# Kernel optimization log

Hardware: AMD Instinct MI355X
Metric: run time of the kernel (lower is better)

## Reference

```python
import jax, jax.numpy as jnp
import numpy as np

HIDDEN = 256
TOPK = 16
SINK_BLOCKS = 5
TAU = 1.0
SOFT_ALPHA = 8.0
LN_EPS = 1e-5


def setup_inputs() -> dict:
    key = jax.random.key(0)
    ks = jax.random.split(key, 8)
    B, T, QD, KD, J = 2, 1024, 1024, 1024, 64
    H = HIDDEN
    H3 = 3 * H
    s = 0.02
    return {
        "Q": jax.random.normal(ks[0], (B, T, QD), dtype=jnp.float32),
        "K": jax.random.normal(ks[1], (B, J, KD), dtype=jnp.float32),
        "Wq": jax.random.normal(ks[2], (H, QD), dtype=jnp.float32) * s,
        "Wk": jax.random.normal(ks[3], (H, KD), dtype=jnp.float32) * s,
        "ln_g": jnp.ones((H3,), dtype=jnp.float32),
        "ln_b": jnp.zeros((H3,), dtype=jnp.float32),
        "Wu": jax.random.normal(ks[4], (H, H3), dtype=jnp.float32) * s,
        "bu": jnp.zeros((H,), dtype=jnp.float32),
        "Wv": jax.random.normal(ks[5], (H, H3), dtype=jnp.float32) * s,
        "bv": jnp.zeros((H,), dtype=jnp.float32),
        "Wo": jax.random.normal(ks[6], (1, H), dtype=jnp.float32) * s,
        "bo": jnp.zeros((1,), dtype=jnp.float32),
        "chunk_len": 16,
        "L_ctx": 1024,
    }


def _forward(Q, K, Wq, Wk, ln_g, ln_b, Wu, bu, Wv, bv, Wo, bo, chunk_len, L_ctx):
    B, T, _ = Q.shape
    J = K.shape[1]
    # ---- GatedScorer ----
    q = jnp.einsum('btd,hd->bth', Q, Wq)  # (B,T,H)
    k = jnp.einsum('bjd,hd->bjh', K, Wk)  # (B,J,H)
    H = q.shape[-1]
    qb = jnp.broadcast_to(q[:, :, None, :], (B, T, J, H))
    kb = jnp.broadcast_to(k[:, None, :, :], (B, T, J, H))
    x = jnp.concatenate([qb, kb, qb * kb], axis=-1)  # (B,T,J,3H)
    mu = jnp.mean(x, axis=-1, keepdims=True)
    var = jnp.mean((x - mu) ** 2, axis=-1, keepdims=True)
    x = (x - mu) / jnp.sqrt(var + LN_EPS) * ln_g + ln_b
    U = jnp.einsum('btjc,hc->btjh', x, Wu) + bu
    V = jnp.einsum('btjc,hc->btjh', x, Wv) + bv
    Z = U * jax.nn.gelu(V, approximate=False)
    logits = jnp.einsum('btjh,oh->btjo', Z, Wo)[..., 0] + bo[0]  # (B,T,J)

    # ---- top-k chunk selection (deterministic path, use_learnable_k=False) ----
    sink = int(min(max(0, SINK_BLOCKS), J))
    J_tail = J - sink
    topk_main = max(min(J, TOPK) - sink, 0)
    logits_tail = logits[..., sink:]  # (B,T,J_tail)
    causal = jnp.arange(J_tail)[None, :] <= jnp.arange(T)[:, None]  # tril(T,J_tail)
    masked = jnp.where(causal[None], logits_tail, -jnp.inf)
    _, idx_tail = jax.lax.top_k(masked, topk_main)
    idx_tail = idx_tail + sink
    sink_idx = jnp.broadcast_to(jnp.arange(sink)[None, None, :], (B, T, sink))
    idx = jnp.concatenate([sink_idx, idx_tail], axis=-1)  # (B,T,sink+topk_main)

    # ---- soft warmup weights ----
    w_soft = jax.nn.softmax(logits / TAU, axis=-1)  # (B,T,J)

    # ---- build_block_bias_from_topk ----
    num_chunks = (L_ctx + chunk_len - 1) // chunk_len
    sel = jnp.zeros((B, T, num_chunks), dtype=bool)
    sel = sel.at[jnp.arange(B)[:, None, None], jnp.arange(T)[None, :, None], idx].set(True)
    token_chunk = jnp.clip(jnp.arange(L_ctx) // chunk_len, 0, num_chunks - 1)  # (L_ctx,)
    sel_tok = jnp.take(sel, token_chunk, axis=-1)  # (B,T,L_ctx)
    per_chunk_bias = -SOFT_ALPHA * (1.0 - w_soft)  # (B,T,J)
    bias = jnp.take(per_chunk_bias, token_chunk, axis=-1)  # (B,T,L_ctx)
    bias = jnp.where(sel_tok, 0.0, bias)
    tri = jnp.arange(L_ctx)[None, :] > jnp.arange(T)[:, None]  # triu(T,L_ctx, diag=1)
    bias = jnp.where(tri[None], -jnp.inf, bias)
    return logits, bias


def reference(Q, K, Wq, Wk, ln_g, ln_b, Wu, bu, Wv, bv, Wo, bo, chunk_len, L_ctx):
    return _forward(Q, K, Wq, Wk, ln_g, ln_b, Wu, bu, Wv, bv, Wo, bo, chunk_len, L_ctx)
```

## Files before the change

kernel.cpp:

```cpp
#include <hip/hip_runtime.h>
#include <hip/hip_bf16.h>
#include <math.h>

#define H3 768

#define OFF_Q     0u
#define OFF_K     524288u
#define OFF_UVK   557056u
#define OFF_SQ    622592u
#define OFF_SQ2   624768u
#define OFF_WGU   626944u
#define OFF_WGV   627200u
#define OFF_CU    627456u
#define OFF_CV    627712u

#define BO_UVQ   0u
#define BO_WQF   1048576u
#define BO_WKF   1310720u
#define BO_BPK   1572864u
#define BO_WQBF  1703936u
#define BO_WKBF  1835008u

typedef __attribute__((ext_vector_type(8))) short bf16x8;
typedef __attribute__((ext_vector_type(4))) float f32x4;

__device__ __forceinline__ float bf2f(short s) {
    return __uint_as_float(((unsigned)(unsigned short)s) << 16);
}
union bfu { __hip_bfloat162 h; short2 s; };
__device__ __forceinline__ void split2(float a, float b, short* hi2, short* lo2) {
    bfu h; h.h = __float22bfloat162_rn(float2{a, b});
    float fa = bf2f(h.s.x), fb = bf2f(h.s.y);
    bfu l; l.h = __float22bfloat162_rn(float2{a - fa, b - fb});
    hi2[0] = h.s.x; hi2[1] = h.s.y;
    lo2[0] = l.s.x; lo2[1] = l.s.y;
}
__device__ __forceinline__ void split8(const float* v, bf16x8* vh, bf16x8* vl) {
    short h2[2], l2[2];
#pragma unroll
    for (int i = 0; i < 4; i++) {
        split2(v[2 * i], v[2 * i + 1], h2, l2);
        (*vh)[2 * i] = h2[0]; (*vh)[2 * i + 1] = h2[1];
        (*vl)[2 * i] = l2[0]; (*vl)[2 * i + 1] = l2[1];
    }
}

__device__ __forceinline__ float gelu_fast(float v) {
    float ar = v * 0.70710678118654752440f;
    float a = fabsf(ar);
    float t = __builtin_amdgcn_rcpf(fmaf(0.3275911f, a, 1.0f));
    float p = fmaf(fmaf(fmaf(fmaf(1.061405429f, t, -1.453152027f), t,
                             1.421413741f), t, -0.284496736f), t, 0.254829592f) * t;
    float e = __expf(-ar * ar);
    float er = fmaf(-p, e, 1.0f);
    er = copysignf(er, ar);
    return 0.5f * v * (1.0f + er);
}

__device__ __forceinline__ float wave_reduce_add(float v) {
#pragma unroll
    for (int off = 32; off > 0; off >>= 1) v += __shfl_xor(v, off, 64);
    return v;
}

__global__ __launch_bounds__(256) void prep(const float* __restrict__ Wq,
                                            const float* __restrict__ Wk,
                                            const float* __restrict__ Wu,
                                            const float* __restrict__ Wv,
                                            const float* __restrict__ g,
                                            const float* __restrict__ lb,
                                            const float* __restrict__ bu,
                                            const float* __restrict__ bv,
                                            float* __restrict__ ws,
                                            float* __restrict__ bsc) {
    int tid = threadIdx.x;
    int bid = blockIdx.x;
    if (bid >= 512) {
        ws[(bid - 512) * 256 + tid] = 0.0f;
        return;
    }
    if (bid < 64) {
        int h = bid * 4 + (tid >> 6);
        int lane = tid & 63;
        float su = 0.f, sv = 0.f, tu = 0.f, tv = 0.f;
#pragma unroll
        for (int i = 0; i < 12; i++) {
            int c = lane + 64 * i;
            float gg = g[c], bb = lb[c];
            float wu = Wu[h * H3 + c], wv = Wv[h * H3 + c];
            su += wu * gg; sv += wv * gg; tu += wu * bb; tv += wv * bb;
        }
        su = wave_reduce_add(su); sv = wave_reduce_add(sv);
        tu = wave_reduce_add(tu); tv = wave_reduce_add(tv);
        if (lane == 0) {
            ws[OFF_WGU + h] = su; ws[OFF_WGV + h] = sv;
            ws[OFF_CU + h] = tu + bu[h]; ws[OFF_CV + h] = tv + bv[h];
        }
        return;
    }
    float v8[8];
    bf16x8 vh, vl;
    if (bid < 320) {
        const float* W; bf16x8* dst;
        int idx;
        if (bid < 192) { idx = (bid - 64) * 256 + tid; W = Wq; dst = (bf16x8*)(bsc + BO_WQF); }
        else { idx = (bid - 192) * 256 + tid; W = Wk; dst = (bf16x8*)(bsc + BO_WKF); }
        int n = idx >> 7, k8 = idx & 127;
        const float* src = W + (size_t)n * 1024 + k8 * 8;
        *(float4*)&v8[0] = *(const float4*)src;
        *(float4*)&v8[4] = *(const float4*)(src + 4);
        split8(v8, &vh, &vl);
        int kc = k8 >> 2, grp = k8 & 3, lane = grp * 16 + (n & 15), ntg = n >> 4;
        size_t s0 = ((size_t)(kc * 16 + ntg) * 2) * 64 + lane;
        dst[s0] = vh; dst[s0 + 64] = vl;
        return;
    }
    int idx, c0;
    bf16x8* dst;
    int n;
    if (bid < 384) {
        idx = (bid - 320) * 256 + tid;
        n = idx >> 5; c0 = (idx & 31) * 8;
        dst = (bf16x8*)(bsc + BO_WQBF);
    } else if (bid < 448) {
        idx = (bid - 384) * 256 + tid;
        n = idx >> 5; c0 = 256 + (idx & 31) * 8;
        dst = (bf16x8*)(bsc + BO_WKBF);
    } else {
        idx = (bid - 448) * 256 + tid;
        n = idx >> 5; c0 = 512 + (idx & 31) * 8;
        dst = (bf16x8*)(bsc + BO_BPK);
    }
    int h, uv;
    if (bid < 448) { uv = (n < 256) ? 0 : 1; h = (n < 256) ? n : n - 256; }
    else {
        int ntg0 = n >> 4, cc = n & 15;
        uv = ntg0 & 1;
        h = ((ntg0 >> 3) << 6) | (((ntg0 >> 1) & 3) << 4) | cc;
    }
    const float* W = uv ? Wv : Wu;
#pragma unroll
    for (int i = 0; i < 8; i++) v8[i] = W[(size_t)h * H3 + c0 + i] * g[c0 + i];
    split8(v8, &vh, &vl);
    int k8 = (c0 & 255) >> 3;
    int kc = k8 >> 2, grp = k8 & 3, lane = grp * 16 + (n & 15), ntg = n >> 4;
    size_t s0 = ((size_t)(kc * 32 + ntg) * 2) * 64 + lane;
    dst[s0] = vh; dst[s0 + 64] = vl;
}

__global__ __launch_bounds__(256) void proj_mfma(const float* __restrict__ Q,
                                                 const float* __restrict__ Kin,
                                                 const float* __restrict__ bsc,
                                                 float* __restrict__ ws) {
    __shared__ __align__(16) short Ah[2][32 * 40], Al[2][32 * 40];
    int tid = threadIdx.x, bx = blockIdx.x, by = blockIdx.y, ks = blockIdx.z;
    const float* A; float* C; const bf16x8* BF;
    if (by < 64) {
        A = Q + (size_t)by * 32 * 1024;
        C = ws + OFF_Q + (size_t)by * 32 * 256;
        BF = (const bf16x8*)(bsc + BO_WQF);
    } else {
        A = Kin + (size_t)(by - 64) * 32 * 1024;
        C = ws + OFF_K + (size_t)(by - 64) * 32 * 256;
        BF = (const bf16x8*)(bsc + BO_WKF);
    }
    int w = tid >> 6, l = tid & 63, c15 = l & 15, grp = l >> 4;
    int mt = w & 1, np = w >> 1;
    int srow = tid >> 3, scol = (tid & 7) * 4;
    const float* arow = A + (size_t)srow * 1024 + ks * 512 + scol;
    f32x4 acc[2];
    acc[0] = (f32x4){0.f, 0.f, 0.f, 0.f};
    acc[1] = (f32x4){0.f, 0.f, 0.f, 0.f};
    float4 a4 = *(const float4*)&arow[0];
    for (int kc = 0; kc < 16; kc++) {
        int pb = kc & 1;
        short h4[4], l4[4];
        split2(a4.x, a4.y, &h4[0], &l4[0]);
        split2(a4.z, a4.w, &h4[2], &l4[2]);
        int ao = srow * 40 + scol;
        *(short4*)&Ah[pb][ao] = *(short4*)&h4[0];
        *(short4*)&Al[pb][ao] = *(short4*)&l4[0];
        if (kc < 15) a4 = *(const float4*)&arow[(kc + 1) * 32];
        __syncthreads();
        int fo = (mt * 16 + c15) * 40 + grp * 8;
        bf16x8 afh = *(const bf16x8*)&Ah[pb][fo];
        bf16x8 afl = *(const bf16x8*)&Al[pb][fo];
        int kcg = ks * 16 + kc;
        bf16x8 bh[2], bl[2];
#pragma unroll
        for (int i = 0; i < 2; i++) {
            int ntg = bx * 4 + 2 * np + i;
            size_t fi = ((size_t)(kcg * 16 + ntg) * 2) * 64 + l;
            bh[i] = BF[fi]; bl[i] = BF[fi + 64];
        }
#pragma unroll
        for (int i = 0; i < 2; i++)
            acc[i] = __builtin_amdgcn_mfma_f32_16x16x32_bf16(afl, bh[i], acc[i], 0, 0, 0);
#pragma unroll
        for (int i = 0; i < 2; i++)
            acc[i] = __builtin_amdgcn_mfma_f32_16x16x32_bf16(afh, bl[i], acc[i], 0, 0, 0);
#pragma unroll
        for (int i = 0; i < 2; i++)
            acc[i] = __builtin_amdgcn_mfma_f32_16x16x32_bf16(afh, bh[i], acc[i], 0, 0, 0);
    }
#pragma unroll
    for (int r = 0; r < 4; r++) {
        int rloc = mt * 16 + grp * 4 + r;
#pragma unroll
        for (int i = 0; i < 2; i++)
            atomicAdd(&C[(size_t)rloc * 256 + bx * 64 + (2 * np + i) * 16 + c15], acc[i][r]);
    }
}

__global__ __launch_bounds__(256) void uv_mfma(float* __restrict__ ws,
                                               float* __restrict__ bsc) {
    __shared__ __align__(16) short Ah[64 * 40], Al[64 * 40];
    int tid = threadIdx.x, bx = blockIdx.x, by = blockIdx.y;
    const float* A; float* C; const bf16x8* BF; int sbase;
    if (by < 32) {
        A = ws + OFF_Q + (size_t)by * 64 * 256;
        C = bsc + BO_UVQ + (size_t)by * 64 * 512;
        BF = (const bf16x8*)(bsc + BO_WQBF);
        sbase = by * 64;
    } else {
        A = ws + OFF_K + (size_t)(by - 32) * 64 * 256;
        C = ws + OFF_UVK + (size_t)(by - 32) * 64 * 512;
        BF = (const bf16x8*)(bsc + BO_WKBF);
        sbase = 2048 + (by - 32) * 64;
    }
    int w = tid >> 6, l = tid & 63, c15 = l & 15, grp = l >> 4;
    int srow = tid >> 2, scol = (tid & 3) * 8;
    f32x4 acc[4];
#pragma unroll
    for (int nt = 0; nt < 4; nt++) acc[nt] = (f32x4){0.f, 0.f, 0.f, 0.f};
    float s1 = 0.f, s2 = 0.f;
    for (int kc = 0; kc < 8; kc++) {
        float v8[8];
        const float* src = &A[(size_t)srow * 256 + kc * 32 + scol];
        *(float4*)&v8[0] = *(const float4*)src;
        *(float4*)&v8[4] = *(const float4*)(src + 4);
        if (bx == 0) {
#pragma unroll
            for (int i = 0; i < 8; i++) { s1 += v8[i]; s2 = fmaf(v8[i], v8[i], s2); }
        }
        bf16x8 vh, vl;
        split8(v8, &vh, &vl);
        int ao = srow * 40 + scol;
        *(bf16x8*)&Ah[ao] = vh;
        *(bf16x8*)&Al[ao] = vl;
        __syncthreads();
        int fo = (w * 16 + c15) * 40 + grp * 8;
        bf16x8 afh = *(const bf16x8*)&Ah[fo];
        bf16x8 afl = *(const bf16x8*)&Al[fo];
        bf16x8 bh[4], bl[4];
#pragma unroll
        for (int nt = 0; nt < 4; nt++) {
            int ntg = bx * 4 + nt;
            size_t fi = ((size_t)(kc * 32 + ntg) * 2) * 64 + l;
            bh[nt] = BF[fi]; bl[nt] = BF[fi + 64];
        }
#pragma unroll
        for (int nt = 0; nt < 4; nt++)
            acc[nt] = __builtin_amdgcn_mfma_f32_16x16x32_bf16(afl, bh[nt], acc[nt], 0, 0, 0);
#pragma unroll
        for (int nt = 0; nt < 4; nt++)
            acc[nt] = __builtin_amdgcn_mfma_f32_16x16x32_bf16(afh, bl[nt], acc[nt], 0, 0, 0);
#pragma unroll
        for (int nt = 0; nt < 4; nt++)
            acc[nt] = __builtin_amdgcn_mfma_f32_16x16x32_bf16(afh, bh[nt], acc[nt], 0, 0, 0);
        __syncthreads();
    }
    if (bx == 0) {
        s1 += __shfl_xor(s1, 1, 64); s1 += __shfl_xor(s1, 2, 64);
        s2 += __shfl_xor(s2, 1, 64); s2 += __shfl_xor(s2, 2, 64);
        if ((tid & 3) == 0) {
            ws[OFF_SQ + sbase + srow] = s1;
            ws[OFF_SQ2 + sbase + srow] = s2;
        }
    }
#pragma unroll
    for (int nt = 0; nt < 4; nt++)
#pragma unroll
        for (int r = 0; r < 4; r++)
            C[(size_t)(w * 16 + grp * 4 + r) * 512 + bx * 64 + nt * 16 + c15] = acc[nt][r];
}

__global__ __launch_bounds__(256, 2) void main_mfma(const float* __restrict__ ws,
                                                    const float* __restrict__ bsc,
                                                    const float* __restrict__ Wo,
                                                    const float* __restrict__ bo,
                                                    float* __restrict__ logits) {
    __shared__ float kk[256];
    __shared__ __align__(16) short Ah[8][64 * 32];
    __shared__ __align__(16) short Al[8][64 * 32];
    __shared__ float mu_s[64], inv_s[64];
    __shared__ float part_s[4][64];
    int tid = threadIdx.x;
    int bidf = blockIdx.x;
    int ti = ((bidf & 7) << 1) | ((bidf >> 3) & 1);
    int j = (bidf >> 4) & 63;
    int b = bidf >> 10;
    int t0 = ti << 6;
    int bj = (b << 6) | j;
    int rot8 = bidf & 7;
    kk[tid] = ws[OFF_K + bj * 256 + tid];
    int w = tid >> 6, l = tid & 63, c15 = l & 15, grp = l >> 4;
    int srow = tid >> 2, scol = (tid & 3) * 8;
    const float* qrow = ws + OFF_Q + (size_t)((b << 10) + t0 + srow) * 256 + scol;
    const bf16x8* bpk = (const bf16x8*)(bsc + BO_BPK);
    const float* UVQ = bsc + BO_UVQ;
    int ntg0 = w * 8;
    float wgu_r[4], wgv_r[4], cu_r[4], cv_r[4], wo_r[4], uk_r[4], vk_r[4];
    int h4[4];
#pragma unroll
    for (int a = 0; a < 4; a++) {
        int h = (w << 6) | (a << 4) | c15;
        h4[a] = h;
        wgu_r[a] = ws[OFF_WGU + h]; wgv_r[a] = ws[OFF_WGV + h];
        cu_r[a] = ws[OFF_CU + h]; cv_r[a] = ws[OFF_CV + h];
        wo_r[a] = Wo[h];
        uk_r[a] = ws[OFF_UVK + (size_t)bj * 512 + h];
        vk_r[a] = ws[OFF_UVK + (size_t)bj * 512 + 256 + h];
    }
    f32x4 acc[4][8];
#pragma unroll
    for (int mt = 0; mt < 4; mt++) {
#pragma unroll
        for (int r4 = 0; r4 < 4; r4++) {
            int row = (b << 10) + t0 + mt * 16 + grp * 4 + r4;
            const float* uvq = UVQ + (size_t)row * 512;
#pragma unroll
            for (int a = 0; a < 4; a++) {
                acc[mt][2 * a][r4]     = uvq[h4[a]] + uk_r[a];
                acc[mt][2 * a + 1][r4] = uvq[256 + h4[a]] + vk_r[a];
            }
        }
    }
    float s1 = 0.f, s2 = 0.f;
    int ao = ((((srow >> 4) << 6) | ((tid & 3) << 4) | (srow & 15)) << 3);
    __syncthreads();
#pragma unroll
    for (int kc = 0; kc < 8; kc++) {
        float q8[8], kv[8];
        *(float4*)&q8[0] = *(const float4*)&qrow[kc * 32];
        *(float4*)&q8[4] = *(const float4*)&qrow[kc * 32 + 4];
        *(float4*)&kv[0] = *(const float4*)&kk[kc * 32 + scol];
        *(float4*)&kv[4] = *(const float4*)&kk[kc * 32 + scol + 4];
        bf16x8 vh, vl;
        short htmp[2], ltmp[2];
#pragma unroll
        for (int i = 0; i < 4; i++) {
            float a = q8[2 * i] * kv[2 * i];
            float c = q8[2 * i + 1] * kv[2 * i + 1];
            s1 += a + c;
            s2 = fmaf(a, a, s2); s2 = fmaf(c, c, s2);
            split2(a, c, htmp, ltmp);
            vh[2 * i] = htmp[0]; vh[2 * i + 1] = htmp[1];
            vl[2 * i] = ltmp[0]; vl[2 * i + 1] = ltmp[1];
        }
        *(bf16x8*)&Ah[kc][ao] = vh;
        *(bf16x8*)&Al[kc][ao] = vl;
    }
    s1 += __shfl_xor(s1, 1, 64); s1 += __shfl_xor(s1, 2, 64);
    s2 += __shfl_xor(s2, 1, 64); s2 += __shfl_xor(s2, 2, 64);
    if ((tid & 3) == 0) {
        int row = (b << 10) + t0 + srow;
        float sq = s1 + ws[OFF_SQ + row] + ws[OFF_SQ + 2048 + bj];
        float sq2 = s2 + ws[OFF_SQ2 + row] + ws[OFF_SQ2 + 2048 + bj];
        float muv = sq * (1.0f / 768.0f);
        float ex2 = sq2 * (1.0f / 768.0f);
        mu_s[srow] = muv;
        inv_s[srow] = 1.0f / sqrtf(ex2 - muv * muv + 1e-5f);
    }
    __syncthreads();
#pragma unroll
    for (int ii = 0; ii < 8; ii++) {
        int kcg = (ii + rot8) & 7;
        bf16x8 afh[4], afl[4];
#pragma unroll
        for (int mt = 0; mt < 4; mt++) {
            int fo = ((mt << 6) | l) << 3;
            afh[mt] = *(const bf16x8*)&Ah[kcg][fo];
            afl[mt] = *(const bf16x8*)&Al[kcg][fo];
        }
        const bf16x8* bpc = bpk + ((size_t)(kcg * 32 + ntg0) * 2) * 64 + l;
#pragma unroll
        for (int nt = 0; nt < 8; nt++) {
            bf16x8 bh = bpc[(size_t)nt * 128];
            bf16x8 bl = bpc[(size_t)nt * 128 + 64];
#pragma unroll
            for (int mt = 0; mt < 4; mt++)
                acc[mt][nt] = __builtin_amdgcn_mfma_f32_16x16x32_bf16(afl[mt], bh, acc[mt][nt], 0, 0, 0);
#pragma unroll
            for (int mt = 0; mt < 4; mt++)
                acc[mt][nt] = __builtin_amdgcn_mfma_f32_16x16x32_bf16(afh[mt], bl, acc[mt][nt], 0, 0, 0);
#pragma unroll
            for (int mt = 0; mt < 4; mt++)
                acc[mt][nt] = __builtin_amdgcn_mfma_f32_16x16x32_bf16(afh[mt], bh, acc[mt][nt], 0, 0, 0);
        }
    }
#pragma unroll
    for (int mt = 0; mt < 4; mt++) {
#pragma unroll
        for (int r4 = 0; r4 < 4; r4++) {
            int r = mt * 16 + grp * 4 + r4;
            float muv = mu_s[r], invv = inv_s[r];
            float part = 0.f;
#pragma unroll
            for (int a = 0; a < 4; a++) {
                float U = fmaf(invv, fmaf(-muv, wgu_r[a], acc[mt][2 * a][r4]), cu_r[a]);
                float V = fmaf(invv, fmaf(-muv, wgv_r[a], acc[mt][2 * a + 1][r4]), cv_r[a]);
                part = fmaf(wo_r[a] * U, gelu_fast(V), part);
            }
            part += __shfl_xor(part, 1, 64);
            part += __shfl_xor(part, 2, 64);
            part += __shfl_xor(part, 4, 64);
            part += __shfl_xor(part, 8, 64);
            if (c15 == 0) part_s[w][r] = part;
        }
    }
    __syncthreads();
    if (tid < 64) {
        float v = bo[0] + part_s[0][tid] + part_s[1][tid] + part_s[2][tid] + part_s[3][tid];
        logits[(size_t)((b << 10) + t0 + tid) * 64 + j] = v;
    }
}

__global__ __launch_bounds__(256) void topk_bias(const float* __restrict__ logits,
                                                 float* __restrict__ bias,
                                                 const int* __restrict__ p_cl,
                                                 const int* __restrict__ p_L) {
    int wv = threadIdx.x >> 6, lane = threadIdx.x & 63;
    int row = blockIdx.x * 4 + wv;
    int t = row & 1023;
    __shared__ float pcb[4][64];
    float L = logits[(size_t)row * 64 + lane];
    float mx = L;
#pragma unroll
    for (int off = 32; off > 0; off >>= 1) mx = fmaxf(mx, __shfl_xor(mx, off, 64));
    float e = expf(L - mx);
    float s = wave_reduce_add(e);
    pcb[wv][lane] = -8.0f * (1.0f - e / s);
    bool valid = (lane >= 5) && ((lane - 5) <= t);
    float val = (lane >= 5) ? (valid ? L : -INFINITY) : -INFINITY;
    int idv = (lane >= 5) ? lane : (1 << 28);
    unsigned long long selmask = 0x1Full;
    for (int it = 0; it < 11; it++) {
        float bv = val; int bi = idv;
#pragma unroll
        for (int off = 32; off > 0; off >>= 1) {
            float ov = __shfl_xor(bv, off, 64);
            int oi = __shfl_xor(bi, off, 64);
            if (ov > bv || (ov == bv && oi < bi)) { bv = ov; bi = oi; }
        }
        selmask |= 1ull << bi;
        if (lane == bi) { val = -INFINITY; idv = (1 << 27); }
    }
    int clen = p_cl[0], Lctx = p_L[0];
    int nch1 = (Lctx + clen - 1) / clen - 1;
    bool p2 = (clen & (clen - 1)) == 0;
    int sh = 31 - __clz(clen);
    float* brow = bias + (size_t)row * Lctx;
    if ((Lctx & 3) == 0) {
        float4* brow4 = (float4*)brow;
        for (int q = lane; q < (Lctx >> 2); q += 64) {
            float o[4];
#pragma unroll
            for (int i = 0; i < 4; i++) {
                int ll = 4 * q + i;
                unsigned cq = p2 ? ((unsigned)ll >> sh) : ((unsigned)ll / (unsigned)clen);
                int c = min(min(cq, (unsigned)nch1), 63u);
                float v;
                if (ll > t) v = -1e30f;
                else if ((selmask >> c) & 1ull) v = 0.0f;
                else v = pcb[wv][c];
                o[i] = v;
            }
            brow4[q] = *(float4*)&o[0];
        }
    } else {
        for (int ll = lane; ll < Lctx; ll += 64) {
            unsigned cq = p2 ? ((unsigned)ll >> sh) : ((unsigned)ll / (unsigned)clen);
            int c = min(min(cq, (unsigned)nch1), 63u);
            float v;
            if (ll > t) v = -1e30f;
            else if ((selmask >> c) & 1ull) v = 0.0f;
            else v = pcb[wv][c];
            brow[ll] = v;
        }
    }
}

extern "C" void kernel_launch(void* const* d_in, const int* in_sizes, int n_in,
                              void* d_out, int out_size, void* d_ws, size_t ws_size,
                              hipStream_t stream) {
    const float* Q   = (const float*)d_in[0];
    const float* Kin = (const float*)d_in[1];
    const float* Wq  = (const float*)d_in[2];
    const float* Wk  = (const float*)d_in[3];
    const float* g   = (const float*)d_in[4];
    const float* lb  = (const float*)d_in[5];
    const float* Wu  = (const float*)d_in[6];
    const float* bu  = (const float*)d_in[7];
    const float* Wv  = (const float*)d_in[8];
    const float* bv  = (const float*)d_in[9];
    const float* Wo  = (const float*)d_in[10];
    const float* bo  = (const float*)d_in[11];
    const int* p_cl  = (const int*)d_in[12];
    const int* p_L   = (const int*)d_in[13];
    float* ws = (float*)d_ws;
    float* logits = (float*)d_out;
    float* bias = (float*)d_out + (size_t)2 * 1024 * 64;

    prep<<<2688, 256, 0, stream>>>(Wq, Wk, Wu, Wv, g, lb, bu, bv, ws, bias);
    proj_mfma<<<dim3(4, 68, 2), 256, 0, stream>>>(Q, Kin, bias, ws);
    uv_mfma<<<dim3(8, 34), 256, 0, stream>>>(ws, bias);
    main_mfma<<<2048, 256, 0, stream>>>(ws, bias, Wo, bo, logits);
    topk_bias<<<512, 256, 0, stream>>>(logits, bias, p_cl, p_L);
}
```

Before: 227.2 us.

## Split main kernel accumulators into two halves and use memset for workspace zeroing

The main MFMA kernel now handles the output columns in two halves of four n-tiles each. It keeps 16 accumulator vectors live instead of 32 and folds each half's U/V gelu epilogue into a running partial sum, which cuts register pressure and may raise occupancy. The price is reading the A fragments from LDS twice. Separately, zeroing the workspace moves out of extra prep blocks into hipMemsetAsync, which adds another operation to the stream.

```diff
diff --git a/kernel.cpp b/kernel.cpp
--- a/kernel.cpp
+++ b/kernel.cpp
@@ -75,10 +75,6 @@
                                             float* __restrict__ bsc) {
     int tid = threadIdx.x;
     int bid = blockIdx.x;
-    if (bid >= 512) {
-        ws[(bid - 512) * 256 + tid] = 0.0f;
-        return;
-    }
     if (bid < 64) {
         int h = bid * 4 + (tid >> 6);
         int lane = tid & 63;
@@ -322,20 +318,6 @@
         uk_r[a] = ws[OFF_UVK + (size_t)bj * 512 + h];
         vk_r[a] = ws[OFF_UVK + (size_t)bj * 512 + 256 + h];
     }
-    f32x4 acc[4][8];
-#pragma unroll
-    for (int mt = 0; mt < 4; mt++) {
-#pragma unroll
-        for (int r4 = 0; r4 < 4; r4++) {
-            int row = (b << 10) + t0 + mt * 16 + grp * 4 + r4;
-            const float* uvq = UVQ + (size_t)row * 512;
-#pragma unroll
-            for (int a = 0; a < 4; a++) {
-                acc[mt][2 * a][r4]     = uvq[h4[a]] + uk_r[a];
-                acc[mt][2 * a + 1][r4] = uvq[256 + h4[a]] + vk_r[a];
-            }
-        }
-    }
     float s1 = 0.f, s2 = 0.f;
     int ao = ((((srow >> 4) << 6) | ((tid & 3) << 4) | (srow & 15)) << 3);
     __syncthreads();
@@ -373,50 +355,80 @@
         inv_s[srow] = 1.0f / sqrtf(ex2 - muv * muv + 1e-5f);
     }
     __syncthreads();
-#pragma unroll
-    for (int ii = 0; ii < 8; ii++) {
-        int kcg = (ii + rot8) & 7;
-        bf16x8 afh[4], afl[4];
+    float part[4][4];
+#pragma unroll
+    for (int mt = 0; mt < 4; mt++)
+#pragma unroll
+        for (int r4 = 0; r4 < 4; r4++) part[mt][r4] = 0.f;
+#pragma unroll
+    for (int half = 0; half < 2; half++) {
+        f32x4 acc[4][4];
 #pragma unroll
         for (int mt = 0; mt < 4; mt++) {
-            int fo = ((mt << 6) | l) << 3;
-            afh[mt] = *(const bf16x8*)&Ah[kcg][fo];
-            afl[mt] = *(const bf16x8*)&Al[kcg][fo];
-        }
-        const bf16x8* bpc = bpk + ((size_t)(kcg * 32 + ntg0) * 2) * 64 + l;
-#pragma unroll
-        for (int nt = 0; nt < 8; nt++) {
-            bf16x8 bh = bpc[(size_t)nt * 128];
-            bf16x8 bl = bpc[(size_t)nt * 128 + 64];
-#pragma unroll
-            for (int mt = 0; mt < 4; mt++)
-                acc[mt][nt] = __builtin_amdgcn_mfma_f32_16x16x32_bf16(afl[mt], bh, acc[mt][nt], 0, 0, 0);
-#pragma unroll
-            for (int mt = 0; mt < 4; mt++)
-                acc[mt][nt] = __builtin_amdgcn_mfma_f32_16x16x32_bf16(afh[mt], bl, acc[mt][nt], 0, 0, 0);
-#pragma unroll
-            for (int mt = 0; mt < 4; mt++)
-                acc[mt][nt] = __builtin_amdgcn_mfma_f32_16x16x32_bf16(afh[mt], bh, acc[mt][nt], 0, 0, 0);
+#pragma unroll
+            for (int r4 = 0; r4 < 4; r4++) {
+                int row = (b << 10) + t0 + mt * 16 + grp * 4 + r4;
+                const float* uvq = UVQ + (size_t)row * 512;
+#pragma unroll
+                for (int al = 0; al < 2; al++) {
+                    int a = half * 2 + al;
+                    acc[mt][2 * al][r4]     = uvq[h4[a]] + uk_r[a];
+                    acc[mt][2 * al + 1][r4] = uvq[256 + h4[a]] + vk_r[a];
+                }
+            }
+        }
+#pragma unroll
+        for (int ii = 0; ii < 8; ii++) {
+            int kcg = (ii + rot8) & 7;
+            bf16x8 afh[4], afl[4];
+#pragma unroll
+            for (int mt = 0; mt < 4; mt++) {
+                int fo = ((mt << 6) | l) << 3;
+                afh[mt] = *(const bf16x8*)&Ah[kcg][fo];
+                afl[mt] = *(const bf16x8*)&Al[kcg][fo];
+            }
+            const bf16x8* bpc = bpk + ((size_t)(kcg * 32 + ntg0 + half * 4) * 2) * 64 + l;
+#pragma unroll
+            for (int ntl = 0; ntl < 4; ntl++) {
+                bf16x8 bh = bpc[(size_t)ntl * 128];
+                bf16x8 bl = bpc[(size_t)ntl * 128 + 64];
+#pragma unroll
+                for (int mt = 0; mt < 4; mt++)
+                    acc[mt][ntl] = __builtin_amdgcn_mfma_f32_16x16x32_bf16(afl[mt], bh, acc[mt][ntl], 0, 0, 0);
+#pragma unroll
+                for (int mt = 0; mt < 4; mt++)
+                    acc[mt][ntl] = __builtin_amdgcn_mfma_f32_16x16x32_bf16(afh[mt], bl, acc[mt][ntl], 0, 0, 0);
+#pragma unroll
+                for (int mt = 0; mt < 4; mt++)
+                    acc[mt][ntl] = __builtin_amdgcn_mfma_f32_16x16x32_bf16(afh[mt], bh, acc[mt][ntl], 0, 0, 0);
+            }
+        }
+#pragma unroll
+        for (int mt = 0; mt < 4; mt++) {
+#pragma unroll
+            for (int r4 = 0; r4 < 4; r4++) {
+                int r = mt * 16 + grp * 4 + r4;
+                float muv = mu_s[r], invv = inv_s[r];
+#pragma unroll
+                for (int al = 0; al < 2; al++) {
+                    int a = half * 2 + al;
+                    float U = fmaf(invv, fmaf(-muv, wgu_r[a], acc[mt][2 * al][r4]), cu_r[a]);
+                    float V = fmaf(invv, fmaf(-muv, wgv_r[a], acc[mt][2 * al + 1][r4]), cv_r[a]);
+                    part[mt][r4] = fmaf(wo_r[a] * U, gelu_fast(V), part[mt][r4]);
+                }
+            }
         }
     }
 #pragma unroll
     for (int mt = 0; mt < 4; mt++) {
 #pragma unroll
         for (int r4 = 0; r4 < 4; r4++) {
-            int r = mt * 16 + grp * 4 + r4;
-            float muv = mu_s[r], invv = inv_s[r];
-            float part = 0.f;
-#pragma unroll
-            for (int a = 0; a < 4; a++) {
-                float U = fmaf(invv, fmaf(-muv, wgu_r[a], acc[mt][2 * a][r4]), cu_r[a]);
-                float V = fmaf(invv, fmaf(-muv, wgv_r[a], acc[mt][2 * a + 1][r4]), cv_r[a]);
-                part = fmaf(wo_r[a] * U, gelu_fast(V), part);
-            }
-            part += __shfl_xor(part, 1, 64);
-            part += __shfl_xor(part, 2, 64);
-            part += __shfl_xor(part, 4, 64);
-            part += __shfl_xor(part, 8, 64);
-            if (c15 == 0) part_s[w][r] = part;
+            float p = part[mt][r4];
+            p += __shfl_xor(p, 1, 64);
+            p += __shfl_xor(p, 2, 64);
+            p += __shfl_xor(p, 4, 64);
+            p += __shfl_xor(p, 8, 64);
+            if (c15 == 0) part_s[w][mt * 16 + grp * 4 + r4] = p;
         }
     }
     __syncthreads();
@@ -512,7 +524,8 @@
     float* logits = (float*)d_out;
     float* bias = (float*)d_out + (size_t)2 * 1024 * 64;
 
-    prep<<<2688, 256, 0, stream>>>(Wq, Wk, Wu, Wv, g, lb, bu, bv, ws, bias);
+    hipMemsetAsync(ws, 0, 557056 * sizeof(float), stream);
+    prep<<<512, 256, 0, stream>>>(Wq, Wk, Wu, Wv, g, lb, bu, bv, ws, bias);
     proj_mfma<<<dim3(4, 68, 2), 256, 0, stream>>>(Q, Kin, bias, ws);
     uv_mfma<<<dim3(8, 34), 256, 0, stream>>>(ws, bias);
     main_mfma<<<2048, 256, 0, stream>>>(ws, bias, Wo, bo, logits);
```

Result: slower. 257.4 us (+13.3%).
